# Performance work log

Measured on AMD Instinct MI355X. Metric: run time of the kernel, lower is better.

The kernel has to match this reference:

```python
import jax, jax.numpy as jnp
import numpy as np

# SCVC config: groups=8, kernel_share=True, kernel_size=3, out_channels=128
N, G, OG, DX, DY = 8, 8, 16, 256, 256  # OG = out_channels // groups


def setup_inputs() -> dict:
    key = jax.random.key(0)
    k = jax.random.split(key, 5)
    return {
        "x": jax.random.normal(k[0], (N, G, DX), dtype=jnp.float32),
        "y": jax.random.normal(k[1], (N, G, DY), dtype=jnp.float32),
        # kernel_C per group: (OG, 1) -> stacked (G, OG); init normal * 3/sqrt(1)
        "C": jax.random.normal(k[2], (G, OG), dtype=jnp.float32) * 3.0,
        # RandomConv1d weights (out=OG, in=1, k=2) per group: stacked (G, OG, 2)
        "wA": jax.random.normal(k[3], (G, OG, 2), dtype=jnp.float32) * 3.0,
        "wB": jax.random.normal(k[4], (G, OG, 2), dtype=jnp.float32) * 3.0,
    }


def _shifted(v):
    # v: (N, G, D). Returns (v[..., p-1], v[..., p+1]) with zero boundaries,
    # which is exactly what pad->dilated conv(k=2, dil=2)->center split computes.
    left = jnp.pad(v, ((0, 0), (0, 0), (1, 0)))[..., :-1]
    right = jnp.pad(v, ((0, 0), (0, 0), (0, 1)))[..., 1:]
    return left, right


def reference(x, y, C, wA, wB):
    # Per-group SCVC (kernel_share=True, 1 channel per group), concat over groups.
    # cross[n,g,o,p,q] = C[g,o] * x[n,g,p] * y[n,g,q]  (batch_cross_product)
    cross = jnp.einsum('go,ngp,ngq->ngopq', C, x, y)
    # dilated-conv correction: a[n,g,o,p] = wA0*x[p-1] + wA1*x[p+1]
    xl, xr = _shifted(x)
    yl, yr = _shifted(y)
    a = (wA[None, :, :, 0, None] * xl[:, :, None, :]
         + wA[None, :, :, 1, None] * xr[:, :, None, :])  # (N, G, OG, DX)
    b = (wB[None, :, :, 0, None] * yl[:, :, None, :]
         + wB[None, :, :, 1, None] * yr[:, :, None, :])  # (N, G, OG, DY)
    out = cross + a[..., :, None] + b[..., None, :]       # (N, G, OG, DX, DY)
    return out.reshape(N, G * OG, DX, DY)
```

## Files before the change

### kernel.cpp

```cpp
#include <hip/hip_runtime.h>


#define N_  8
#define G_  8
#define OG_ 16
#define DX_ 256
#define DY_ 256

typedef float vfloat4 __attribute__((ext_vector_type(4)));

__global__ __launch_bounds__(256) void scvc_kernel(
    const float* __restrict__ x,
    const float* __restrict__ y,
    const float* __restrict__ C,
    const float* __restrict__ wA,
    const float* __restrict__ wB,
    float* __restrict__ out)
{
    __shared__ float sarr[DX_];
    __shared__ float aarr[DX_];
    __shared__ float ybuf[DY_];
    __shared__ float bbuf[DY_];

    const int t    = blockIdx.x >> 1;
    const int half = blockIdx.x & 1;
    const int n   = t / (G_ * OG_);
    const int rem = t % (G_ * OG_);
    const int g   = rem / OG_;
    const int o   = rem % OG_;

    const int tid = threadIdx.x;

    const int go = g * OG_ + o;
    const float co  = C[go];
    const float wa0 = wA[go * 2 + 0];
    const float wa1 = wA[go * 2 + 1];
    const float wb0 = wB[go * 2 + 0];
    const float wb1 = wB[go * 2 + 1];

    const float* xrow = x + (size_t)(n * G_ + g) * DX_;
    const float* yrow = y + (size_t)(n * G_ + g) * DY_;

    {
        float xv = xrow[tid];
        float xl = (tid > 0)       ? xrow[tid - 1] : 0.0f;
        float xr = (tid < DX_ - 1) ? xrow[tid + 1] : 0.0f;
        sarr[tid] = co * xv;
        aarr[tid] = wa0 * xl + wa1 * xr;

        float yv = yrow[tid];
        float yl = (tid > 0)       ? yrow[tid - 1] : 0.0f;
        float yr = (tid < DY_ - 1) ? yrow[tid + 1] : 0.0f;
        ybuf[tid] = yv;
        bbuf[tid] = wb0 * yl + wb1 * yr;
    }
    __syncthreads();

    const int qv = tid & 63;
    const int wv = tid >> 6;
    const int p0 = half * (DX_ / 2) + wv * 32;

    const vfloat4 y4 = ((const vfloat4*)ybuf)[qv];
    const vfloat4 b4 = ((const vfloat4*)bbuf)[qv];

    float* obase = out + (size_t)t * (DX_ * DY_) + (size_t)p0 * DY_;

#pragma unroll 4
    for (int i = 0; i < 32; ++i) {
        const int p  = p0 + i;
        const float s  = sarr[p];
        const float av = aarr[p];
        vfloat4 v;
        v.x = fmaf(s, y4.x, av + b4.x);
        v.y = fmaf(s, y4.y, av + b4.y);
        v.z = fmaf(s, y4.z, av + b4.z);
        v.w = fmaf(s, y4.w, av + b4.w);
        ((vfloat4*)(obase + (size_t)i * DY_))[qv] = v;
    }
}

extern "C" void kernel_launch(void* const* d_in, const int* in_sizes, int n_in,
                              void* d_out, int out_size, void* d_ws, size_t ws_size,
                              hipStream_t stream) {
    const float* x  = (const float*)d_in[0];
    const float* y  = (const float*)d_in[1];
    const float* C  = (const float*)d_in[2];
    const float* wA = (const float*)d_in[3];
    const float* wB = (const float*)d_in[4];
    float* out = (float*)d_out;

    const int nblocks = N_ * G_ * OG_ * 2;
    scvc_kernel<<<nblocks, 256, 0, stream>>>(x, y, C, wA, wB, out);
}
```

Measured before the change: 255.4 us.

## Drop shared memory and grid-stride output rows across wavefronts

Removes the shared-memory staging and block barrier. Each wavefront now computes whole output rows directly from global x/y, using lane shuffles for the y neighbours, and loops over 32 rows strided across the whole grid. This changes the work split from two blocks per (n,g,o) plane to a fixed 2048-block grid with interleaved rows, and adds a launch-bounds occupancy hint. It trades the one-time LDS staging for redundant per-row global loads of x, y and the weights, which should mostly hit in cache, aiming for a better-spread store stream.

Result: slower. 286.7 us (+12.2%).

```diff
diff --git a/kernel.cpp b/kernel.cpp
--- a/kernel.cpp
+++ b/kernel.cpp
@@ -9,7 +9,7 @@
 
 typedef float vfloat4 __attribute__((ext_vector_type(4)));
 
-__global__ __launch_bounds__(256) void scvc_kernel(
+__global__ __launch_bounds__(256, 8) void scvc_kernel(
     const float* __restrict__ x,
     const float* __restrict__ y,
     const float* __restrict__ C,
@@ -17,65 +17,50 @@
     const float* __restrict__ wB,
     float* __restrict__ out)
 {
-    __shared__ float sarr[DX_];
-    __shared__ float aarr[DX_];
-    __shared__ float ybuf[DY_];
-    __shared__ float bbuf[DY_];
+    const int tid = threadIdx.x;
+    const int qv  = tid & 63;
+    const int wg  = (blockIdx.x << 2) | (tid >> 6);
 
-    const int t    = blockIdx.x >> 1;
-    const int half = blockIdx.x & 1;
-    const int n   = t / (G_ * OG_);
-    const int rem = t % (G_ * OG_);
-    const int g   = rem / OG_;
-    const int o   = rem % OG_;
+    vfloat4* out4 = (vfloat4*)out;
 
-    const int tid = threadIdx.x;
+#pragma unroll 2
+    for (int i = 0; i < 32; ++i) {
+        const int r  = (i << 13) + wg;
+        const int t  = r >> 8;
+        const int p  = r & 255;
+        const int ng = t >> 4;
+        const int go = t & 127;
 
-    const int go = g * OG_ + o;
-    const float co  = C[go];
-    const float wa0 = wA[go * 2 + 0];
-    const float wa1 = wA[go * 2 + 1];
-    const float wb0 = wB[go * 2 + 0];
-    const float wb1 = wB[go * 2 + 1];
+        const float  co  = C[go];
+        const float2 wa  = ((const float2*)wA)[go];
+        const float2 wb  = ((const float2*)wB)[go];
+        const float* xrow = x + ng * DX_;
+        const float xv = xrow[p];
+        const float xl = (p > 0)        ? xrow[p - 1] : 0.0f;
+        const float xr = (p < DX_ - 1)  ? xrow[p + 1] : 0.0f;
 
-    const float* xrow = x + (size_t)(n * G_ + g) * DX_;
-    const float* yrow = y + (size_t)(n * G_ + g) * DY_;
+        const float s  = co * xv;
+        const float av = fmaf(wa.x, xl, wa.y * xr);
 
-    {
-        float xv = xrow[tid];
-        float xl = (tid > 0)       ? xrow[tid - 1] : 0.0f;
-        float xr = (tid < DX_ - 1) ? xrow[tid + 1] : 0.0f;
-        sarr[tid] = co * xv;
-        aarr[tid] = wa0 * xl + wa1 * xr;
+        const vfloat4 y4 = *(const vfloat4*)(y + ng * DY_ + (qv << 2));
+        float ylm = __shfl_up(y4.w, 1);
+        if (qv == 0) ylm = 0.0f;
+        float yrp = __shfl_down(y4.x, 1);
+        if (qv == 63) yrp = 0.0f;
 
-        float yv = yrow[tid];
-        float yl = (tid > 0)       ? yrow[tid - 1] : 0.0f;
-        float yr = (tid < DY_ - 1) ? yrow[tid + 1] : 0.0f;
-        ybuf[tid] = yv;
-        bbuf[tid] = wb0 * yl + wb1 * yr;
-    }
-    __syncthreads();
+        vfloat4 b4;
+        b4.x = fmaf(wb.x, ylm,  wb.y * y4.y);
+        b4.y = fmaf(wb.x, y4.x, wb.y * y4.z);
+        b4.z = fmaf(wb.x, y4.y, wb.y * y4.w);
+        b4.w = fmaf(wb.x, y4.z, wb.y * yrp);
 
-    const int qv = tid & 63;
-    const int wv = tid >> 6;
-    const int p0 = half * (DX_ / 2) + wv * 32;
-
-    const vfloat4 y4 = ((const vfloat4*)ybuf)[qv];
-    const vfloat4 b4 = ((const vfloat4*)bbuf)[qv];
-
-    float* obase = out + (size_t)t * (DX_ * DY_) + (size_t)p0 * DY_;
-
-#pragma unroll 4
-    for (int i = 0; i < 32; ++i) {
-        const int p  = p0 + i;
-        const float s  = sarr[p];
-        const float av = aarr[p];
         vfloat4 v;
         v.x = fmaf(s, y4.x, av + b4.x);
         v.y = fmaf(s, y4.y, av + b4.y);
         v.z = fmaf(s, y4.z, av + b4.z);
         v.w = fmaf(s, y4.w, av + b4.w);
-        ((vfloat4*)(obase + (size_t)i * DY_))[qv] = v;
+
+        out4[(size_t)r * 64 + qv] = v;
     }
 }
 
@@ -89,6 +74,6 @@
     const float* wB = (const float*)d_in[4];
     float* out = (float*)d_out;
 
-    const int nblocks = N_ * G_ * OG_ * 2;
+    const int nblocks = 2048;
     scvc_kernel<<<nblocks, 256, 0, stream>>>(x, y, C, wA, wB, out);
 }
```

## Use persistent-style blocks each producing four full output planes

Applied to the files above, without the earlier changes.

The grid shrinks from 2048 blocks, each writing half a plane, to 256 blocks that each loop over four (n,g,o) planes and write whole 256x256 planes. Each wave now writes 64 rows per plane, and the inner loop unrolls by 8. The aim is to cut block launch and setup overhead and give each block longer streaming store runs. The cost is fewer waves in flight, 256 blocks on a 256-CU device, so a purely store-bound kernel may lose latency hiding. Each iteration also adds a barrier and an x/y reload.

Measured after the change: 260.0 us. Within noise of the previous version (+1.8%).

```diff
diff --git a/kernel.cpp b/kernel.cpp
--- a/kernel.cpp
+++ b/kernel.cpp
@@ -22,60 +22,54 @@
     __shared__ float ybuf[DY_];
     __shared__ float bbuf[DY_];
 
-    const int t    = blockIdx.x >> 1;
-    const int half = blockIdx.x & 1;
-    const int n   = t / (G_ * OG_);
-    const int rem = t % (G_ * OG_);
-    const int g   = rem / OG_;
-    const int o   = rem % OG_;
+    const int tid = threadIdx.x;
+    const int qv  = tid & 63;
+    const int wv  = tid >> 6;
 
-    const int tid = threadIdx.x;
+    for (int j = 0; j < 4; ++j) {
+        const int t  = (blockIdx.x << 2) | j;
+        const int go = t & 127;
+        const int ng = ((t >> 7) << 3) | (go >> 4);
 
-    const int go = g * OG_ + o;
-    const float co  = C[go];
-    const float wa0 = wA[go * 2 + 0];
-    const float wa1 = wA[go * 2 + 1];
-    const float wb0 = wB[go * 2 + 0];
-    const float wb1 = wB[go * 2 + 1];
+        __syncthreads();
+        {
+            const float  co = C[go];
+            const float2 wa = ((const float2*)wA)[go];
+            const float2 wb = ((const float2*)wB)[go];
+            const float* xrow = x + ng * DX_;
+            const float* yrow = y + ng * DY_;
 
-    const float* xrow = x + (size_t)(n * G_ + g) * DX_;
-    const float* yrow = y + (size_t)(n * G_ + g) * DY_;
+            float xv = xrow[tid];
+            float xl = (tid > 0)       ? xrow[tid - 1] : 0.0f;
+            float xr = (tid < DX_ - 1) ? xrow[tid + 1] : 0.0f;
+            sarr[tid] = co * xv;
+            aarr[tid] = fmaf(wa.x, xl, wa.y * xr);
 
-    {
-        float xv = xrow[tid];
-        float xl = (tid > 0)       ? xrow[tid - 1] : 0.0f;
-        float xr = (tid < DX_ - 1) ? xrow[tid + 1] : 0.0f;
-        sarr[tid] = co * xv;
-        aarr[tid] = wa0 * xl + wa1 * xr;
+            float yv = yrow[tid];
+            float yl = (tid > 0)       ? yrow[tid - 1] : 0.0f;
+            float yr = (tid < DY_ - 1) ? yrow[tid + 1] : 0.0f;
+            ybuf[tid] = yv;
+            bbuf[tid] = fmaf(wb.x, yl, wb.y * yr);
+        }
+        __syncthreads();
 
-        float yv = yrow[tid];
-        float yl = (tid > 0)       ? yrow[tid - 1] : 0.0f;
-        float yr = (tid < DY_ - 1) ? yrow[tid + 1] : 0.0f;
-        ybuf[tid] = yv;
-        bbuf[tid] = wb0 * yl + wb1 * yr;
-    }
-    __syncthreads();
+        const vfloat4 y4 = ((const vfloat4*)ybuf)[qv];
+        const vfloat4 b4 = ((const vfloat4*)bbuf)[qv];
 
-    const int qv = tid & 63;
-    const int wv = tid >> 6;
-    const int p0 = half * (DX_ / 2) + wv * 32;
+        float* obase = out + (size_t)t * (DX_ * DY_) + (size_t)(wv * 64) * DY_;
 
-    const vfloat4 y4 = ((const vfloat4*)ybuf)[qv];
-    const vfloat4 b4 = ((const vfloat4*)bbuf)[qv];
-
-    float* obase = out + (size_t)t * (DX_ * DY_) + (size_t)p0 * DY_;
-
-#pragma unroll 4
-    for (int i = 0; i < 32; ++i) {
-        const int p  = p0 + i;
-        const float s  = sarr[p];
-        const float av = aarr[p];
-        vfloat4 v;
-        v.x = fmaf(s, y4.x, av + b4.x);
-        v.y = fmaf(s, y4.y, av + b4.y);
-        v.z = fmaf(s, y4.z, av + b4.z);
-        v.w = fmaf(s, y4.w, av + b4.w);
-        ((vfloat4*)(obase + (size_t)i * DY_))[qv] = v;
+#pragma unroll 8
+        for (int i = 0; i < 64; ++i) {
+            const int p  = (wv << 6) + i;
+            const float s  = sarr[p];
+            const float av = aarr[p];
+            vfloat4 v;
+            v.x = fmaf(s, y4.x, av + b4.x);
+            v.y = fmaf(s, y4.y, av + b4.y);
+            v.z = fmaf(s, y4.z, av + b4.z);
+            v.w = fmaf(s, y4.w, av + b4.w);
+            ((vfloat4*)(obase + (size_t)i * DY_))[qv] = v;
+        }
     }
 }
 
@@ -89,6 +83,6 @@
     const float* wB = (const float*)d_in[4];
     float* out = (float*)d_out;
 
-    const int nblocks = N_ * G_ * OG_ * 2;
+    const int nblocks = 256;
     scvc_kernel<<<nblocks, 256, 0, stream>>>(x, y, C, wA, wB, out);
 }
```
